# Performance work log

Hardware: AMD Instinct MI355X
Metric: run time of the kernel (lower is better)

The kernel has to match this reference:

```python
import jax, jax.numpy as jnp
import numpy as np

N_LAYERS = 3
FEATS = 128
POS = 3
M_DIM = 64
E_IN = 1 + 2 * FEATS          # 257 (rel_dist + x_i + x_j)
N_NODES = 20000
N_EDGES = 320000
LN_EPS = 1e-5


def _xavier(key, shape):
    fan_in, fan_out = shape[0], shape[1]
    std = (2.0 / (fan_in + fan_out)) ** 0.5
    return jax.random.normal(key, shape, dtype=jnp.float32) * std


def setup_inputs() -> dict:
    key = jax.random.key(0)
    ks = jax.random.split(key, 10)
    x = jax.random.normal(ks[0], (N_NODES, POS + FEATS), dtype=jnp.float32)
    edge_index = jax.random.randint(ks[1], (2, N_EDGES), 0, N_NODES)
    L = N_LAYERS
    def stack(k, shape):
        return jax.vmap(lambda kk: _xavier(kk, shape))(jax.random.split(k, L))
    params = {
        "ew1": stack(ks[2], (E_IN, 2 * E_IN)),      # edge_mlp linear 1
        "eb1": jnp.zeros((L, 2 * E_IN), jnp.float32),
        "ew2": stack(ks[3], (2 * E_IN, M_DIM)),      # edge_mlp linear 2
        "eb2": jnp.zeros((L, M_DIM), jnp.float32),
        "ng": jnp.ones((L, FEATS), jnp.float32),     # node LayerNorm gamma
        "nb": jnp.zeros((L, FEATS), jnp.float32),    # node LayerNorm beta
        "nw1": stack(ks[4], (FEATS + M_DIM, 2 * FEATS)),
        "nb1": jnp.zeros((L, 2 * FEATS), jnp.float32),
        "nw2": stack(ks[5], (2 * FEATS, FEATS)),
        "nb2": jnp.zeros((L, FEATS), jnp.float32),
        "cw1": stack(ks[6], (M_DIM, 4 * M_DIM)),
        "cb1": jnp.zeros((L, 4 * M_DIM), jnp.float32),
        "cw2": stack(ks[7], (4 * M_DIM, 1)),
        "cb2": jnp.zeros((L, 1), jnp.float32),
    }
    return {"x": x, "edge_index": edge_index, **params}


def _layer(x, edge_index, ew1, eb1, ew2, eb2, ng, nb, nw1, nb1, nw2, nb2,
           cw1, cb1, cw2, cb2):
    coors, feats = x[:, :POS], x[:, POS:]
    src, dst = edge_index[0], edge_index[1]
    # relative geometry per edge
    rel_coors = coors[src] - coors[dst]                       # [E, 3]
    rel_dist = jnp.sum(rel_coors * rel_coors, axis=-1, keepdims=True)  # [E, 1]
    # message MLP: cat[x_i (target), x_j (source), rel_dist]
    e_in = jnp.concatenate([feats[dst], feats[src], rel_dist], axis=-1)
    h = jax.nn.silu(e_in @ ew1 + eb1)
    m_ij = jax.nn.silu(h @ ew2 + eb2)                         # [E, m_dim]
    # coordinate update
    coor_w = jax.nn.silu(m_ij @ cw1 + cb1) @ cw2 + cb2        # [E, 1]
    mhat = jax.ops.segment_sum(coor_w * rel_coors, dst, num_segments=N_NODES)
    coors_out = coors + mhat
    # feature update (LayerNorm then MLP, residual)
    m_i = jax.ops.segment_sum(m_ij, dst, num_segments=N_NODES)
    mu = jnp.mean(feats, axis=-1, keepdims=True)
    var = jnp.mean((feats - mu) ** 2, axis=-1, keepdims=True)
    feats_n = (feats - mu) * jax.lax.rsqrt(var + LN_EPS) * ng + nb
    n_in = jnp.concatenate([feats_n, m_i], axis=-1)
    nh = jax.nn.silu(n_in @ nw1 + nb1) @ nw2 + nb2
    feats_out = feats + nh
    return jnp.concatenate([coors_out, feats_out], axis=-1)


def reference(x, edge_index, ew1, eb1, ew2, eb2, ng, nb, nw1, nb1, nw2, nb2,
              cw1, cb1, cw2, cb2):
    for l in range(N_LAYERS):
        x = _layer(x, edge_index,
                   ew1[l], eb1[l], ew2[l], eb2[l],
                   ng[l], nb[l], nw1[l], nb1[l], nw2[l], nb2[l],
                   cw1[l], cb1[l], cw2[l], cb2[l])
    return x
```

## Files before the change

kernel.cpp:

```cpp
#include <hip/hip_runtime.h>

typedef unsigned short u16;
typedef unsigned int   u32;
typedef __attribute__((ext_vector_type(2))) u32  u32x2;
typedef __attribute__((ext_vector_type(4))) u32  u32x4;
typedef __attribute__((ext_vector_type(8))) __bf16 bf16x8;
typedef __attribute__((ext_vector_type(4))) float  f32x4;

#define NN 20000
#define NE 320000
#define XD 131
#define F  128
#define MD 64
#define H1 514
#define H1P 544
#define NCH 17

#define GAS __attribute__((address_space(1)))
#define LAS __attribute__((address_space(3)))
#define LGKM0 asm volatile("s_waitcnt lgkmcnt(0)" ::: "memory")
#define VM0   asm volatile("s_waitcnt vmcnt(0)" ::: "memory")

__device__ __forceinline__ float silu(float a) {
    float e = __expf(-a);
    return a * __builtin_amdgcn_rcpf(1.0f + e);
}

__device__ __forceinline__ u16 f2bf(float f) {
    u32 u = __builtin_bit_cast(u32, f);
    return (u16)((u + 0x7FFFu + ((u >> 16) & 1u)) >> 16);
}
__device__ __forceinline__ u16 bfc(float f) { return __builtin_bit_cast(u16, (__bf16)f); }
__device__ __forceinline__ u32 pk2(float a, float b) {
    return (u32)bfc(a) | ((u32)bfc(b) << 16);
}
__device__ __forceinline__ float blo(u32 u) { return __builtin_bit_cast(float, u << 16); }
__device__ __forceinline__ float bhi(u32 u) { return __builtin_bit_cast(float, u & 0xFFFF0000u); }
__device__ __forceinline__ bf16x8 mk8(u32 a, u32 b, u32 c, u32 d) {
    u32x4 t = {a, b, c, d};
    return __builtin_bit_cast(bf16x8, t);
}
__device__ __forceinline__ f32x4 mfma16(bf16x8 a, bf16x8 b, f32x4 c) {
    return __builtin_amdgcn_mfma_f32_16x16x32_bf16(a, b, c, 0, 0, 0);
}


__global__ void prep_w1o(const float* __restrict__ ew1, const float* __restrict__ eb1,
                         u16* __restrict__ w1b, float* __restrict__ bias2) {
    int i = blockIdx.x * 256 + threadIdx.x;
    if (i >= 3 * H1P * 256) return;
    int k = i & 255;
    int n = (i >> 8) % H1P;
    int l = (i >> 8) / H1P;
    float v = (n < H1) ? ew1[(size_t)l * 257 * H1 + (size_t)k * H1 + n] : 0.f;
    w1b[(size_t)(l * H1P + n) * 256 + (k ^ ((n & 7) << 3))] = f2bf(v);
    if (k == 0) {
        bias2[(l * H1P + n) * 2 + 0] = (n < H1) ? eb1[l * H1 + n] : 0.f;
        bias2[(l * H1P + n) * 2 + 1] = (n < H1) ? ew1[(size_t)l * 257 * H1 + (size_t)256 * H1 + n] : 0.f;
    }
}

__global__ void prep_w1n(const float* __restrict__ ew1, const float* __restrict__ eb1,
                         u16* __restrict__ w1p, float* __restrict__ eb1p, float* __restrict__ w1lf) {
    int i = blockIdx.x * 256 + threadIdx.x;
    if (i >= 3 * 1088 * 128) return;
    int k = i & 127;
    int n = (i >> 7) % 1088;
    int l = (i >> 7) / 1088;
    float v;
    if (n < H1P) v = (n < H1) ? ew1[(size_t)l * 257 * H1 + (size_t)k * H1 + n] : 0.f;
    else { int nn = n - H1P; v = (nn < H1) ? ew1[(size_t)l * 257 * H1 + (size_t)(128 + k) * H1 + nn] : 0.f; }
    w1p[(size_t)(l * 1088 + n) * 128 + k] = f2bf(v);
    if (k == 0 && n < H1P) {
        eb1p[l * H1P + n] = (n < H1) ? eb1[l * H1 + n] : 0.f;
        w1lf[l * H1P + n] = (n < H1) ? ew1[(size_t)l * 257 * H1 + (size_t)256 * H1 + n] : 0.f;
    }
}

__global__ void prep_w2(const float* __restrict__ ew2, u16* __restrict__ w2b) {
    int i = blockIdx.x * 256 + threadIdx.x;
    if (i >= 3 * 64 * H1P) return;
    int k = i % H1P;
    int n = (i / H1P) & 63;
    int l = i / (H1P * 64);
    float v = (k < H1) ? ew2[(size_t)l * H1 * 64 + (size_t)k * 64 + n] : 0.f;
    w2b[(size_t)(l * 64 + n) * H1P + k] = f2bf(v);
}

__global__ void prep_cw1(const float* __restrict__ cw1, u16* __restrict__ cw1b) {
    int i = blockIdx.x * 256 + threadIdx.x;
    if (i >= 3 * 256 * 64) return;
    int k = i & 63;
    int n = (i >> 6) & 255;
    int l = i >> 14;
    cw1b[(size_t)l * 16384 + n * 64 + k] = f2bf(cw1[(size_t)l * 16384 + k * 256 + n]);
}

__global__ void prep_nw1(const float* __restrict__ nw1, u16* __restrict__ nw1b) {
    int i = blockIdx.x * 256 + threadIdx.x;
    if (i >= 3 * 256 * 192) return;
    int k = i % 192;
    int n = (i / 192) & 255;
    int l = i / (192 * 256);
    nw1b[(size_t)(l * 256 + n) * 192 + k] = f2bf(nw1[(size_t)l * 192 * 256 + (size_t)k * 256 + n]);
}

__global__ void prep_nw2(const float* __restrict__ nw2, u16* __restrict__ nw2b) {
    int i = blockIdx.x * 256 + threadIdx.x;
    if (i >= 3 * 128 * 256) return;
    int k = i & 255;
    int n = (i >> 8) & 127;
    int l = i >> 15;
    nw2b[(size_t)(l * 128 + n) * 256 + k] = f2bf(nw2[(size_t)l * 256 * 128 + (size_t)k * 128 + n]);
}

__global__ void x2bf(const float* __restrict__ xc, u32* __restrict__ xbf) {
    int i = blockIdx.x * 256 + threadIdx.x;
    if (i >= NN * 64) return;
    const int node = i >> 6, p = i & 63;
    const float a = xc[(size_t)node * XD + 3 + 2 * p];
    const float b = xc[(size_t)node * XD + 4 + 2 * p];
    xbf[(size_t)node * 64 + p] = pk2(a, b);
}


__global__ __launch_bounds__(256, 4) void ygemm(
    const u16* __restrict__ xbf, const char* __restrict__ w1p,
    const float* __restrict__ eb1p, u16* __restrict__ Y)
{
    const int tid = threadIdx.x;
    const int w = tid >> 6, l = tid & 63, lg = l >> 4, lc = l & 15;
    const int nb0 = blockIdx.x * 128 + w * 32;
    const int n0 = nb0 + lc, n1 = nb0 + 16 + lc;
    const bool v0 = n0 < NN, v1 = n1 < NN;
    const int m0 = v0 ? n0 : NN - 1, m1 = v1 ? n1 : NN - 1;

    bf16x8 BF[2][4];
    #pragma unroll
    for (int kt = 0; kt < 4; ++kt) {
        BF[0][kt] = *(const bf16x8*)((const char*)xbf + (size_t)m0 * 256 + kt * 64 + lg * 16);
        BF[1][kt] = *(const bf16x8*)((const char*)xbf + (size_t)m1 * 256 + kt * 64 + lg * 16);
    }

    const int t0 = blockIdx.y * 17;
    #pragma unroll 1
    for (int t = t0; t < t0 + 17; ++t) {
        bf16x8 AW[4];
        #pragma unroll
        for (int kt = 0; kt < 4; ++kt)
            AW[kt] = *(const bf16x8*)(w1p + (size_t)(t * 16 + lc) * 256 + kt * 64 + lg * 16);
        const int cb = t * 16 + lg * 4;
        f32x4 binit = {0.f, 0.f, 0.f, 0.f};
        if (cb < H1P) binit = *(const f32x4*)(eb1p + cb);
        f32x4 c0 = binit, c1 = binit;
        #pragma unroll
        for (int kt = 0; kt < 4; ++kt) {
            c0 = mfma16(AW[kt], BF[0][kt], c0);
            c1 = mfma16(AW[kt], BF[1][kt], c1);
        }
        u32x2 p0, p1;
        p0[0] = pk2(c0[0], c0[1]); p0[1] = pk2(c0[2], c0[3]);
        p1[0] = pk2(c1[0], c1[1]); p1[1] = pk2(c1[2], c1[3]);
        if (v0) *(u32x2*)(Y + (size_t)m0 * 1088 + cb) = p0;
        if (v1) *(u32x2*)(Y + (size_t)m1 * 1088 + cb) = p1;
    }
}


__global__ void csr_hist(const int* __restrict__ eidx, int* __restrict__ cnt) {
    int e = blockIdx.x * 256 + threadIdx.x;
    if (e < NE) atomicAdd(&cnt[eidx[NE + e]], 1);
}

__global__ void csr_scan(const int* __restrict__ cnt, int* __restrict__ rowp) {
    __shared__ int ps[1024];
    const int t = threadIdx.x;
    const int base = t * 20;
    int loc[20];
    int s = 0;
    #pragma unroll
    for (int i = 0; i < 20; ++i) {
        const int idx = base + i;
        const int c = (idx < NN) ? cnt[idx] : 0;
        loc[i] = s;
        s += c;
    }
    ps[t] = s;
    __syncthreads();
    for (int off = 1; off < 1024; off <<= 1) {
        int v = (t >= off) ? ps[t - off] : 0;
        __syncthreads();
        ps[t] += v;
        __syncthreads();
    }
    const int segbase = (t > 0) ? ps[t - 1] : 0;
    #pragma unroll
    for (int i = 0; i < 20; ++i) {
        const int idx = base + i;
        if (idx < NN) rowp[idx] = segbase + loc[i];
    }
    if (t == 1023) rowp[NN] = ps[1023];
}

__global__ void csr_fill(const int* __restrict__ eidx, const int* __restrict__ rowp,
                         int* __restrict__ fill, int* __restrict__ eids) {
    int e = blockIdx.x * 256 + threadIdx.x;
    if (e >= NE) return;
    const int d = eidx[NE + e];
    const int pos = atomicAdd(&fill[d], 1);
    eids[rowp[d] + pos] = e;
}

__global__ void esort(const int* __restrict__ eidx, const int* __restrict__ eids,
                      int* __restrict__ esrc, int* __restrict__ edst) {
    int j = blockIdx.x * 256 + threadIdx.x;
    if (j >= NE) return;
    const int e = eids[j];
    esrc[j] = eidx[e];
    edst[j] = eidx[NE + e];
}


__global__ __launch_bounds__(256, 4) void reduce_mi(
    const u16* __restrict__ gmij, const float* __restrict__ gmh,
    const int* __restrict__ rowp, float* __restrict__ m_i, float* __restrict__ mh) {
    const int tid = threadIdx.x;
    const int n = blockIdx.x * 8 + (tid >> 5);
    const int t = tid & 31;
    if (n >= NN) return;
    const int b = rowp[n], e = rowp[n + 1];
    float a0 = 0.f, a1 = 0.f;
    for (int j = b; j < e; ++j) {
        const u32 v = *(const u32*)(gmij + (size_t)j * 64 + t * 2);
        a0 += blo(v);
        a1 += bhi(v);
    }
    m_i[(size_t)n * 64 + 2 * t]     = a0;
    m_i[(size_t)n * 64 + 2 * t + 1] = a1;
    if (t < 3) {
        float m = 0.f;
        for (int j = b; j < e; ++j) m += gmh[(size_t)j * 4 + t];
        mh[n * 3 + t] = m;
    }
}


__global__ __launch_bounds__(256, 4) void edge_mfma2(
    const float* __restrict__ x, const u16* __restrict__ Y,
    const int* __restrict__ esrc, const int* __restrict__ edst,
    const float* __restrict__ w1lf,
    const char* __restrict__ w2b, const float* __restrict__ eb2,
    const char* __restrict__ cw1b, const float* __restrict__ cb1,
    const float* __restrict__ cw2, const float* __restrict__ cb2,
    u16* __restrict__ gmij, float* __restrict__ gmh)
{
    __shared__ __align__(16) char LDS[19456];
    const int tid = threadIdx.x;
    const int w = tid >> 6, l = tid & 63, lg = l >> 4, lc = l & 15;
    const int ebase = blockIdx.x * 128 + w * 32;
    char*  MJ  = LDS + w * 4352;
    float* RDS = (float*)(LDS + 17408);

    if (l < 32) {
        const int e = ebase + l;
        const int s = esrc[e], d = edst[e];
        const float ax = x[(size_t)s * XD + 0] - x[(size_t)d * XD + 0];
        const float ay = x[(size_t)s * XD + 1] - x[(size_t)d * XD + 1];
        const float az = x[(size_t)s * XD + 2] - x[(size_t)d * XD + 2];
        f32x4 v = {ax, ay, az, ax * ax + ay * ay + az * az};
        *(f32x4*)(RDS + (w * 32 + l) * 4) = v;
    }
    const int s0 = esrc[ebase + lc],      d0 = edst[ebase + lc];
    const int s1 = esrc[ebase + 16 + lc], d1 = edst[ebase + 16 + lc];
    LGKM0;
    const float rd0 = RDS[(w * 32 + lc) * 4 + 3];
    const float rd1 = RDS[(w * 32 + 16 + lc) * 4 + 3];

    f32x4 c2[2][4];
    #pragma unroll
    for (int nt = 0; nt < 4; ++nt) {
        const float b = eb2[nt * 16 + lc];
        c2[0][nt] = (f32x4){b, b, b, b};
        c2[1][nt] = (f32x4){b, b, b, b};
    }

    #pragma unroll 1
    for (int ch = 0; ch < NCH; ++ch) {
        const int cb = ch * 32 + lg * 8;
        u32x4 ya0 = *(const u32x4*)(Y + (size_t)d0 * 1088 + cb);
        u32x4 yb0 = *(const u32x4*)(Y + (size_t)s0 * 1088 + 544 + cb);
        u32x4 ya1 = *(const u32x4*)(Y + (size_t)d1 * 1088 + cb);
        u32x4 yb1 = *(const u32x4*)(Y + (size_t)s1 * 1088 + 544 + cb);
        f32x4 wlA = *(const f32x4*)(w1lf + cb);
        f32x4 wlB = *(const f32x4*)(w1lf + cb + 4);
        u32 pk0[4], pk1[4];
        #pragma unroll
        for (int j = 0; j < 4; ++j) {
            const float wa = (j < 2) ? wlA[2 * j]     : wlB[2 * j - 4];
            const float wb = (j < 2) ? wlA[2 * j + 1] : wlB[2 * j - 3];
            {
                const float a0 = blo(ya0[j]) + blo(yb0[j]) + rd0 * wa;
                const float a1 = bhi(ya0[j]) + bhi(yb0[j]) + rd0 * wb;
                pk0[j] = pk2(silu(a0), silu(a1));
            }
            {
                const float a0 = blo(ya1[j]) + blo(yb1[j]) + rd1 * wa;
                const float a1 = bhi(ya1[j]) + bhi(yb1[j]) + rd1 * wb;
                pk1[j] = pk2(silu(a0), silu(a1));
            }
        }
        bf16x8 A20 = mk8(pk0[0], pk0[1], pk0[2], pk0[3]);
        bf16x8 A21 = mk8(pk1[0], pk1[1], pk1[2], pk1[3]);
        #pragma unroll
        for (int nt = 0; nt < 4; ++nt) {
            bf16x8 Bw = __builtin_bit_cast(bf16x8,
                *(const u32x4*)(w2b + (size_t)(nt * 16 + lc) * 1088 + ch * 64 + lg * 16));
            c2[0][nt] = mfma16(A20, Bw, c2[0][nt]);
            c2[1][nt] = mfma16(A21, Bw, c2[1][nt]);
        }
    }

    #pragma unroll
    for (int mt = 0; mt < 2; ++mt)
        #pragma unroll
        for (int nt = 0; nt < 4; ++nt)
            #pragma unroll
            for (int r = 0; r < 4; ++r) {
                const float v = silu(c2[mt][nt][r]);
                const int rowl = mt * 16 + lg * 4 + r;
                const int col  = nt * 16 + lc;
                *(u16*)(MJ + rowl * 136 + col * 2) = bfc(v);
            }
    LGKM0;

    {
        u16* grow = gmij + (size_t)ebase * 64;
        #pragma unroll
        for (int i = 0; i < 4; ++i) {
            const int row = i * 8 + (l >> 3);
            u32x4 v = *(u32x4*)(MJ + row * 136 + (l & 7) * 16);
            *(u32x4*)(grow + (size_t)row * 64 + (l & 7) * 8) = v;
        }
    }

    bf16x8 A3[2][2];
    #pragma unroll
    for (int mt = 0; mt < 2; ++mt)
        #pragma unroll
        for (int kt = 0; kt < 2; ++kt)
            A3[mt][kt] = *(bf16x8*)(MJ + (mt * 16 + lc) * 136 + kt * 64 + lg * 16);

    float pw[2][4] = {{0.f, 0.f, 0.f, 0.f}, {0.f, 0.f, 0.f, 0.f}};
    #pragma unroll 4
    for (int ct3 = 0; ct3 < 16; ++ct3) {
        const int col = ct3 * 16 + lc;
        const float b = cb1[col];
        f32x4 c30 = {b, b, b, b}, c31 = {b, b, b, b};
        #pragma unroll
        for (int kt = 0; kt < 2; ++kt) {
            bf16x8 B = __builtin_bit_cast(bf16x8,
                *(const u32x4*)(cw1b + (size_t)col * 128 + kt * 64 + lg * 16));
            c30 = mfma16(A3[0][kt], B, c30);
            c31 = mfma16(A3[1][kt], B, c31);
        }
        const float w2v = cw2[col];
        #pragma unroll
        for (int r = 0; r < 4; ++r) {
            pw[0][r] = fmaf(silu(c30[r]), w2v, pw[0][r]);
            pw[1][r] = fmaf(silu(c31[r]), w2v, pw[1][r]);
        }
    }
    #pragma unroll
    for (int m = 1; m < 16; m <<= 1)
        #pragma unroll
        for (int mt = 0; mt < 2; ++mt)
            #pragma unroll
            for (int r = 0; r < 4; ++r)
                pw[mt][r] += __shfl_xor(pw[mt][r], m, 64);

    const float cb2v = cb2[0];
    if (lc < 3) {
        #pragma unroll
        for (int mt = 0; mt < 2; ++mt)
            #pragma unroll
            for (int r = 0; r < 4; ++r) {
                const int rowl = mt * 16 + lg * 4 + r;
                const float cwv = pw[mt][r] + cb2v;
                gmh[(size_t)(ebase + rowl) * 4 + lc] = cwv * RDS[(w * 32 + rowl) * 4 + lc];
            }
    }
}


__global__ __launch_bounds__(256, 3) void edge_mfma(
    const float* __restrict__ x, const u16* __restrict__ xbf,
    const int* __restrict__ esrc, const int* __restrict__ edst,
    const char* __restrict__ w1b, const float* __restrict__ bias2,
    const char* __restrict__ w2b, const float* __restrict__ eb2,
    const char* __restrict__ cw1b, const float* __restrict__ cb1,
    const float* __restrict__ cw2, const float* __restrict__ cb2,
    float* __restrict__ m_i, float* __restrict__ mhat,
    u16* __restrict__ gmij, float* __restrict__ gmh)
{
    __shared__ __align__(16) char LDS[45568];
    const int tid = threadIdx.x;
    const int w = tid >> 6, l = tid & 63, lg = l >> 4, lc = l & 15;
    const int ebase = blockIdx.x * 128 + w * 32;
    char*  HT  = LDS + 32768 + w * 2560;
    char*  MJ  = LDS + w * 4352;
    float* RDS = (float*)(LDS + 43008);
    int*   SDS = (int*)(LDS + 45056);
    char*  STG = LDS + w * 8192;

    if (l < 32) {
        const int e = ebase + l;
        const int s = esrc[e], d = edst[e];
        const float ax = x[(size_t)s * XD + 0] - x[(size_t)d * XD + 0];
        const float ay = x[(size_t)s * XD + 1] - x[(size_t)d * XD + 1];
        const float az = x[(size_t)s * XD + 2] - x[(size_t)d * XD + 2];
        f32x4 v = {ax, ay, az, ax * ax + ay * ay + az * az};
        *(f32x4*)(RDS + (w * 32 + l) * 4) = v;
        SDS[w * 32 + l] = d;
    }

    bf16x8 A[2][8];
    const int r4 = l >> 4;
    #pragma unroll
    for (int p = 0; p < 2; ++p) {
        const int* ea = p ? esrc : edst;
        #pragma unroll
        for (int j = 0; j < 8; ++j) {
            const int r = j * 4 + r4;
            const int node = ea[ebase + r];
            const int cp = lc ^ (r & 7);
            __builtin_amdgcn_global_load_lds((const GAS u32*)(xbf + (size_t)node * 128 + cp * 8),
                                             (LAS u32*)(STG + j * 1024), 16, 0, 0);
        }
        VM0;
        #pragma unroll
        for (int kt = 0; kt < 4; ++kt)
            #pragma unroll
            for (int et = 0; et < 2; ++et) {
                const int R = et * 16 + lc;
                A[et][p * 4 + kt] = *(bf16x8*)(STG + R * 256 + ((kt * 64 + lg * 16) ^ ((R & 7) << 4)));
            }
        LGKM0;
    }

    float rd_e[2];
    rd_e[0] = RDS[(w * 32 + lc) * 4 + 3];
    rd_e[1] = RDS[(w * 32 + 16 + lc) * 4 + 3];
    LGKM0;

    __syncthreads();

    f32x4 c2[2][4];
    #pragma unroll
    for (int nt = 0; nt < 4; ++nt) {
        const float b = eb2[nt * 16 + lc];
        c2[0][nt] = (f32x4){b, b, b, b};
        c2[1][nt] = (f32x4){b, b, b, b};
    }

    {
        const char* g = w1b + (size_t)w * 4096;
        #pragma unroll
        for (int r = 0; r < 4; ++r)
            __builtin_amdgcn_global_load_lds((const GAS u32*)(g + r * 1024 + l * 16),
                                             (LAS u32*)(LDS + w * 4096 + r * 1024), 16, 0, 0);
    }

    const float* pB = bias2;
    #pragma unroll 1
    for (int ch = 0; ch < NCH; ++ch) {
        VM0;
        __syncthreads();
        if (ch + 1 < NCH) {
            const char* g = w1b + (size_t)(ch + 1) * 16384 + w * 4096;
            char* dst = LDS + ((ch + 1) & 1) * 16384 + w * 4096;
            #pragma unroll
            for (int r = 0; r < 4; ++r)
                __builtin_amdgcn_global_load_lds((const GAS u32*)(g + r * 1024 + l * 16),
                                                 (LAS u32*)(dst + r * 1024), 16, 0, 0);
        }
        char* Bc = LDS + (ch & 1) * 16384;

        #pragma unroll
        for (int nt = 0; nt < 2; ++nt) {
            const float* bp = pB + (nt * 16 + lg * 4) * 2;
            f32x4 q0 = *(const f32x4*)(bp);
            f32x4 q1 = *(const f32x4*)(bp + 4);
            f32x4 c10, c11;
            c10[0] = fmaf(rd_e[0], q0[1], q0[0]); c10[1] = fmaf(rd_e[0], q0[3], q0[2]);
            c10[2] = fmaf(rd_e[0], q1[1], q1[0]); c10[3] = fmaf(rd_e[0], q1[3], q1[2]);
            c11[0] = fmaf(rd_e[1], q0[1], q0[0]); c11[1] = fmaf(rd_e[1], q0[3], q0[2]);
            c11[2] = fmaf(rd_e[1], q1[1], q1[0]); c11[3] = fmaf(rd_e[1], q1[3], q1[2]);
            const int nl = nt * 16 + lc;
            #pragma unroll
            for (int kt = 0; kt < 8; ++kt) {
                bf16x8 Wf = *(bf16x8*)(Bc + nl * 512 + ((kt * 64 + lg * 16) ^ ((nl & 7) << 4)));
                c10 = mfma16(Wf, A[0][kt], c10);
                c11 = mfma16(Wf, A[1][kt], c11);
            }
            u32x2 v0, v1;
            v0[0] = pk2(silu(c10[0]), silu(c10[1])); v0[1] = pk2(silu(c10[2]), silu(c10[3]));
            v1[0] = pk2(silu(c11[0]), silu(c11[1])); v1[1] = pk2(silu(c11[2]), silu(c11[3]));
            *(u32x2*)(HT + lc * 80 + nt * 32 + lg * 8) = v0;
            *(u32x2*)(HT + (16 + lc) * 80 + nt * 32 + lg * 8) = v1;
        }
        LGKM0;
        bf16x8 A2[2];
        A2[0] = *(bf16x8*)(HT + lc * 80 + lg * 16);
        A2[1] = *(bf16x8*)(HT + (16 + lc) * 80 + lg * 16);
        #pragma unroll
        for (int nt = 0; nt < 4; ++nt) {
            bf16x8 Bw = __builtin_bit_cast(bf16x8,
                *(const u32x4*)(w2b + (size_t)(nt * 16 + lc) * 1088 + ch * 64 + lg * 16));
            c2[0][nt] = mfma16(A2[0], Bw, c2[0][nt]);
            c2[1][nt] = mfma16(A2[1], Bw, c2[1][nt]);
        }
        pB += 64;
    }

    __syncthreads();

    int dstn[2][4];
    #pragma unroll
    for (int mt = 0; mt < 2; ++mt)
        #pragma unroll
        for (int r = 0; r < 4; ++r)
            dstn[mt][r] = SDS[w * 32 + mt * 16 + lg * 4 + r];

    #pragma unroll
    for (int mt = 0; mt < 2; ++mt)
        #pragma unroll
        for (int nt = 0; nt < 4; ++nt)
            #pragma unroll
            for (int r = 0; r < 4; ++r) {
                const float v = silu(c2[mt][nt][r]);
                const int rowl = mt * 16 + lg * 4 + r;
                const int col  = nt * 16 + lc;
                *(u16*)(MJ + rowl * 136 + col * 2) = bfc(v);
                if (!gmij) atomicAdd(m_i + (size_t)dstn[mt][r] * 64 + col, v);
            }
    LGKM0;

    if (gmij) {
        u16* grow = gmij + (size_t)ebase * 64;
        #pragma unroll
        for (int i = 0; i < 4; ++i) {
            const int row = i * 8 + (l >> 3);
            u32x4 v = *(u32x4*)(MJ + row * 136 + (l & 7) * 16);
            *(u32x4*)(grow + (size_t)row * 64 + (l & 7) * 8) = v;
        }
    }

    bf16x8 A3[2][2];
    #pragma unroll
    for (int mt = 0; mt < 2; ++mt)
        #pragma unroll
        for (int kt = 0; kt < 2; ++kt)
            A3[mt][kt] = *(bf16x8*)(MJ + (mt * 16 + lc) * 136 + kt * 64 + lg * 16);

    float pw[2][4] = {{0.f, 0.f, 0.f, 0.f}, {0.f, 0.f, 0.f, 0.f}};
    #pragma unroll 4
    for (int ct3 = 0; ct3 < 16; ++ct3) {
        const int col = ct3 * 16 + lc;
        const float b = cb1[col];
        f32x4 c30 = {b, b, b, b}, c31 = {b, b, b, b};
        #pragma unroll
        for (int kt = 0; kt < 2; ++kt) {
            bf16x8 B = __builtin_bit_cast(bf16x8,
                *(const u32x4*)(cw1b + (size_t)col * 128 + kt * 64 + lg * 16));
            c30 = mfma16(A3[0][kt], B, c30);
            c31 = mfma16(A3[1][kt], B, c31);
        }
        const float w2v = cw2[col];
        #pragma unroll
        for (int r = 0; r < 4; ++r) {
            pw[0][r] = fmaf(silu(c30[r]), w2v, pw[0][r]);
            pw[1][r] = fmaf(silu(c31[r]), w2v, pw[1][r]);
        }
    }
    #pragma unroll
    for (int m = 1; m < 16; m <<= 1)
        #pragma unroll
        for (int mt = 0; mt < 2; ++mt)
            #pragma unroll
            for (int r = 0; r < 4; ++r)
                pw[mt][r] += __shfl_xor(pw[mt][r], m, 64);

    const float cb2v = cb2[0];
    if (lc < 3) {
        #pragma unroll
        for (int mt = 0; mt < 2; ++mt)
            #pragma unroll
            for (int r = 0; r < 4; ++r) {
                const int rowl = mt * 16 + lg * 4 + r;
                const float cwv = pw[mt][r] + cb2v;
                const float contrib = cwv * RDS[(w * 32 + rowl) * 4 + lc];
                if (gmij)
                    gmh[(size_t)(ebase + rowl) * 4 + lc] = contrib;
                else
                    atomicAdd(mhat + (size_t)dstn[mt][r] * 3 + lc, contrib);
            }
    }
}


__global__ __launch_bounds__(256, 2) void node_mfma(
    const float* __restrict__ xc, const float* __restrict__ m_i, const float* __restrict__ mh,
    const float* __restrict__ ng, const float* __restrict__ nb,
    const char* __restrict__ nw1b, const float* __restrict__ nb1,
    const char* __restrict__ nw2b, const float* __restrict__ nb2,
    float* __restrict__ xn)
{
    __shared__ __align__(16) char LDS[4 * 4352];
    const int tid = threadIdx.x;
    const int w = tid >> 6, l = tid & 63, lg = l >> 4, lc = l & 15;
    char* HB = LDS + w * 4352;
    const int nb0 = blockIdx.x * 128 + w * 32;

    int nodes[2]; bool valid[2];
    #pragma unroll
    for (int et = 0; et < 2; ++et) {
        int n = nb0 + et * 16 + lc;
        valid[et] = (n < NN);
        nodes[et] = valid[et] ? n : (NN - 1);
    }

    bf16x8 BF[2][6];
    #pragma unroll
    for (int et = 0; et < 2; ++et) {
        const float* xr = xc + (size_t)nodes[et] * XD + 3;
        float v[4][8];
        float s = 0.f, q = 0.f;
        #pragma unroll
        for (int kt = 0; kt < 4; ++kt) {
            const int k0 = kt * 32 + lg * 8;
            #pragma unroll
            for (int j = 0; j < 8; ++j) {
                const float t = xr[k0 + j];
                v[kt][j] = t; s += t; q = fmaf(t, t, q);
            }
        }
        s += __shfl_xor(s, 16, 64); s += __shfl_xor(s, 32, 64);
        q += __shfl_xor(q, 16, 64); q += __shfl_xor(q, 32, 64);
        const float mu = s * (1.f / 128.f);
        const float rs = rsqrtf(q * (1.f / 128.f) - mu * mu + 1e-5f);
        #pragma unroll
        for (int kt = 0; kt < 4; ++kt) {
            const int k0 = kt * 32 + lg * 8;
            float4 g0 = *(const float4*)(ng + k0), g1 = *(const float4*)(ng + k0 + 4);
            float4 b0 = *(const float4*)(nb + k0), b1 = *(const float4*)(nb + k0 + 4);
            const u32 u0 = pk2((v[kt][0] - mu) * rs * g0.x + b0.x, (v[kt][1] - mu) * rs * g0.y + b0.y);
            const u32 u1 = pk2((v[kt][2] - mu) * rs * g0.z + b0.z, (v[kt][3] - mu) * rs * g0.w + b0.w);
            const u32 u2 = pk2((v[kt][4] - mu) * rs * g1.x + b1.x, (v[kt][5] - mu) * rs * g1.y + b1.y);
            const u32 u3 = pk2((v[kt][6] - mu) * rs * g1.z + b1.z, (v[kt][7] - mu) * rs * g1.w + b1.w);
            BF[et][kt] = mk8(u0, u1, u2, u3);
        }
        const float* mr = m_i + (size_t)nodes[et] * 64;
        #pragma unroll
        for (int kt2 = 0; kt2 < 2; ++kt2) {
            float4 a = *(const float4*)(mr + kt2 * 32 + lg * 8);
            float4 b = *(const float4*)(mr + kt2 * 32 + lg * 8 + 4);
            BF[et][4 + kt2] = mk8(pk2(a.x, a.y), pk2(a.z, a.w), pk2(b.x, b.y), pk2(b.z, b.w));
        }
    }

    f32x4 a2[8][2];
    #pragma unroll
    for (int ct2 = 0; ct2 < 8; ++ct2) {
        f32x4 b = *(const f32x4*)(nb2 + ct2 * 16 + lg * 4);
        a2[ct2][0] = b; a2[ct2][1] = b;
    }

    #pragma unroll 1
    for (int g = 0; g < 4; ++g) {
        f32x4 a1[4][2];
        #pragma unroll
        for (int ct = 0; ct < 4; ++ct) {
            f32x4 b = *(const f32x4*)(nb1 + g * 64 + ct * 16 + lg * 4);
            a1[ct][0] = b; a1[ct][1] = b;
        }
        #pragma unroll
        for (int ct = 0; ct < 4; ++ct)
            #pragma unroll
            for (int kt = 0; kt < 6; ++kt) {
                bf16x8 Aw = __builtin_bit_cast(bf16x8, *(const u32x4*)(
                    nw1b + (size_t)(g * 64 + ct * 16 + lc) * 384 + kt * 64 + lg * 16));
                a1[ct][0] = mfma16(Aw, BF[0][kt], a1[ct][0]);
                a1[ct][1] = mfma16(Aw, BF[1][kt], a1[ct][1]);
            }
        #pragma unroll
        for (int ct = 0; ct < 4; ++ct)
            #pragma unroll
            for (int et = 0; et < 2; ++et) {
                f32x4 c = a1[ct][et];
                u32 v0 = pk2(silu(c[0]), silu(c[1]));
                u32 v1 = pk2(silu(c[2]), silu(c[3]));
                *(u32*)(HB + (et * 16 + lc) * 136 + ct * 32 + lg * 8) = v0;
                *(u32*)(HB + (et * 16 + lc) * 136 + ct * 32 + lg * 8 + 4) = v1;
            }
        LGKM0;
        __builtin_amdgcn_sched_barrier(0);
        bf16x8 B2[2][2];
        #pragma unroll
        for (int et = 0; et < 2; ++et)
            #pragma unroll
            for (int kt2 = 0; kt2 < 2; ++kt2) {
                u32 a = *(u32*)(HB + (et * 16 + lc) * 136 + kt2 * 64 + lg * 16);
                u32 b = *(u32*)(HB + (et * 16 + lc) * 136 + kt2 * 64 + lg * 16 + 4);
                u32 c = *(u32*)(HB + (et * 16 + lc) * 136 + kt2 * 64 + lg * 16 + 8);
                u32 d = *(u32*)(HB + (et * 16 + lc) * 136 + kt2 * 64 + lg * 16 + 12);
                B2[et][kt2] = mk8(a, b, c, d);
            }
        #pragma unroll
        for (int ct2 = 0; ct2 < 8; ++ct2)
            #pragma unroll
            for (int kt2 = 0; kt2 < 2; ++kt2) {
                bf16x8 Aw = __builtin_bit_cast(bf16x8, *(const u32x4*)(
                    nw2b + (size_t)(ct2 * 16 + lc) * 512 + (g * 64 + kt2 * 32 + lg * 8) * 2));
                a2[ct2][0] = mfma16(Aw, B2[0][kt2], a2[ct2][0]);
                a2[ct2][1] = mfma16(Aw, B2[1][kt2], a2[ct2][1]);
            }
        LGKM0;
        __builtin_amdgcn_sched_barrier(0);
    }

    #pragma unroll
    for (int et = 0; et < 2; ++et) {
        if (!valid[et]) continue;
        const size_t nr = (size_t)nodes[et] * XD;
        #pragma unroll
        for (int ct2 = 0; ct2 < 8; ++ct2)
            #pragma unroll
            for (int r = 0; r < 4; ++r) {
                const int col = ct2 * 16 + lg * 4 + r;
                xn[nr + 3 + col] = a2[ct2][et][r] + xc[nr + 3 + col];
            }
    }
    for (int idx = tid; idx < 384; idx += 256) {
        const int n = blockIdx.x * 128 + idx / 3;
        const int d = idx - (idx / 3) * 3;
        if (n < NN)
            xn[(size_t)n * XD + d] = xc[(size_t)n * XD + d] + mh[n * 3 + d];
    }
}


extern "C" void kernel_launch(void* const* d_in, const int* in_sizes, int n_in,
                              void* d_out, int out_size, void* d_ws, size_t ws_size,
                              hipStream_t stream) {
    const float* x_in = (const float*)d_in[0];
    const int*   eidx = (const int*)  d_in[1];
    const float* ew1  = (const float*)d_in[2];
    const float* eb1  = (const float*)d_in[3];
    const float* ew2  = (const float*)d_in[4];
    const float* eb2  = (const float*)d_in[5];
    const float* ng   = (const float*)d_in[6];
    const float* nb   = (const float*)d_in[7];
    const float* nw1  = (const float*)d_in[8];
    const float* nb1  = (const float*)d_in[9];
    const float* nw2  = (const float*)d_in[10];
    const float* nb2  = (const float*)d_in[11];
    const float* cw1  = (const float*)d_in[12];
    const float* cb1  = (const float*)d_in[13];
    const float* cw2  = (const float*)d_in[14];
    const float* cb2  = (const float*)d_in[15];
    float* out = (float*)d_out;

    char* ws = (char*)d_ws;
    size_t off = 0;
    auto alloc = [&](size_t bytes) { char* p = ws + off; off = (off + bytes + 255) & ~255ull; return p; };
    float* mi    = (float*)alloc((size_t)NN * MD * 4);
    float* mh    = (float*)alloc((size_t)NN * 3 * 4);
    u32*   xbf   = (u32*)  alloc((size_t)NN * 256);
    float* bias2 = (float*)alloc((size_t)3 * H1P * 8);
    float* eb1pf = (float*)alloc((size_t)3 * H1P * 4);
    float* w1lf  = (float*)alloc((size_t)3 * H1P * 4);
    char*  w1b   = alloc((size_t)3 * H1P * 512);
    char*  w1p   = alloc((size_t)3 * 1088 * 256);
    char*  w2b   = alloc((size_t)3 * 64 * 1088);
    char*  cw1b  = alloc((size_t)3 * 256 * 128);
    char*  nw1b  = alloc((size_t)3 * 256 * 384);
    char*  nw2b  = alloc((size_t)3 * 128 * 512);
    int* rowp = (int*) alloc((size_t)(NN + 1) * 4);
    int* eids = (int*) alloc((size_t)NE * 4);
    int* esrc = (int*) alloc((size_t)NE * 4);
    int* edst = (int*) alloc((size_t)NE * 4);
    int* cnt  = (int*) alloc((size_t)NN * 4);
    int* fillp= (int*) alloc((size_t)NN * 4);
    u16* gmij = (u16*)alloc((size_t)NE * 64 * 2);
    float* gmh= (float*)alloc((size_t)NE * 4 * 4);
    const size_t off_two = off;
    u16* Ybuf = (u16*)alloc((size_t)NN * 1088 * 2);
    const size_t off_all = off;
    const bool pathA = (off_all <= ws_size);
    const bool two   = (off_two <= ws_size);

    prep_w1o<<<(3 * H1P * 256 + 255) / 256, 256, 0, stream>>>(ew1, eb1, (u16*)w1b, bias2);
    prep_w1n<<<(3 * 1088 * 128 + 255) / 256, 256, 0, stream>>>(ew1, eb1, (u16*)w1p, eb1pf, w1lf);
    prep_w2 <<<(3 * 64 * H1P + 255) / 256, 256, 0, stream>>>(ew2, (u16*)w2b);
    prep_cw1<<<(3 * 256 * 64 + 255) / 256, 256, 0, stream>>>(cw1, (u16*)cw1b);
    prep_nw1<<<(3 * 256 * 192 + 255) / 256, 256, 0, stream>>>(nw1, (u16*)nw1b);
    prep_nw2<<<(3 * 128 * 256 + 255) / 256, 256, 0, stream>>>(nw2, (u16*)nw2b);

    const int* esrcA = eidx;
    const int* edstA = eidx + NE;
    if (two) {
        hipMemsetAsync(cnt,  0, (size_t)NN * 4, stream);
        hipMemsetAsync(fillp,0, (size_t)NN * 4, stream);
        csr_hist<<<(NE + 255) / 256, 256, 0, stream>>>(eidx, cnt);
        csr_scan<<<1, 1024, 0, stream>>>(cnt, rowp);
        csr_fill<<<(NE + 255) / 256, 256, 0, stream>>>(eidx, rowp, fillp, eids);
        esort<<<(NE + 255) / 256, 256, 0, stream>>>(eidx, eids, esrc, edst);
        esrcA = esrc; edstA = edst;
    }

    for (int l = 0; l < 3; ++l) {
        const float* xc = (l == 0) ? x_in : out;
        float*       xn = out;
        if (!two) {
            hipMemsetAsync(mi, 0, (size_t)NN * MD * 4, stream);
            hipMemsetAsync(mh, 0, (size_t)NN * 3 * 4, stream);
        }
        x2bf<<<(NN * 64 + 255) / 256, 256, 0, stream>>>(xc, xbf);
        if (pathA) {
            ygemm<<<dim3((NN + 127) / 128, 4), 256, 0, stream>>>(
                (const u16*)xbf, w1p + (size_t)l * 1088 * 256, eb1pf + (size_t)l * H1P, Ybuf);
            edge_mfma2<<<NE / 128, 256, 0, stream>>>(
                xc, Ybuf, esrcA, edstA, w1lf + (size_t)l * H1P,
                w2b + (size_t)l * 64 * 1088, eb2 + (size_t)l * 64,
                cw1b + (size_t)l * 256 * 128, cb1 + (size_t)l * 256,
                cw2 + (size_t)l * 256, cb2 + l, gmij, gmh);
            reduce_mi<<<(NN + 7) / 8, 256, 0, stream>>>(gmij, gmh, rowp, mi, mh);
        } else {
            edge_mfma<<<NE / 128, 256, 0, stream>>>(
                xc, (const u16*)xbf, esrcA, edstA,
                w1b + (size_t)l * H1P * 512, bias2 + (size_t)l * H1P * 2,
                w2b + (size_t)l * 64 * 1088, eb2 + (size_t)l * 64,
                cw1b + (size_t)l * 256 * 128, cb1 + (size_t)l * 256,
                cw2 + (size_t)l * 256, cb2 + l,
                mi, mh, two ? gmij : (u16*)nullptr, two ? gmh : (float*)nullptr);
            if (two)
                reduce_mi<<<(NN + 7) / 8, 256, 0, stream>>>(gmij, gmh, rowp, mi, mh);
        }
        node_mfma<<<(NN + 127) / 128, 256, 0, stream>>>(
            xc, mi, mh,
            ng + (size_t)l * F, nb + (size_t)l * F,
            nw1b + (size_t)l * 256 * 384, nb1 + (size_t)l * 256,
            nw2b + (size_t)l * 128 * 512, nb2 + (size_t)l * F,
            xn);
    }
}
```

Baseline: 821.3 us.

## Prefetch next Y chunk in edge kernel and swizzle blocks across XCDs

```diff
diff --git a/kernel.cpp b/kernel.cpp
--- a/kernel.cpp
+++ b/kernel.cpp
@@ -123,7 +123,6 @@
     xbf[(size_t)node * 64 + p] = pk2(a, b);
 }
 
-
 __global__ __launch_bounds__(256, 4) void ygemm(
     const u16* __restrict__ xbf, const char* __restrict__ w1p,
     const float* __restrict__ eb1p, u16* __restrict__ Y)
@@ -257,7 +256,10 @@
     __shared__ __align__(16) char LDS[19456];
     const int tid = threadIdx.x;
     const int w = tid >> 6, l = tid & 63, lg = l >> 4, lc = l & 15;
-    const int ebase = blockIdx.x * 128 + w * 32;
+    const int bx = blockIdx.x;
+    const int xcd = bx & 7, ib = bx >> 3;
+    const int swb = (xcd < 4 ? xcd * 313 : 1252 + (xcd - 4) * 312) + ib;
+    const int ebase = swb * 128 + w * 32;
     char*  MJ  = LDS + w * 4352;
     float* RDS = (float*)(LDS + 17408);
 
@@ -284,15 +286,29 @@
         c2[1][nt] = (f32x4){b, b, b, b};
     }
 
+    const u16* ya0p = Y + (size_t)d0 * 1088;
+    const u16* yb0p = Y + (size_t)s0 * 1088 + 544;
+    const u16* ya1p = Y + (size_t)d1 * 1088;
+    const u16* yb1p = Y + (size_t)s1 * 1088 + 544;
+    const int co = lg * 8;
+
+    u32x4 ya0 = *(const u32x4*)(ya0p + co);
+    u32x4 yb0 = *(const u32x4*)(yb0p + co);
+    u32x4 ya1 = *(const u32x4*)(ya1p + co);
+    u32x4 yb1 = *(const u32x4*)(yb1p + co);
+    f32x4 wlA = *(const f32x4*)(w1lf + co);
+    f32x4 wlB = *(const f32x4*)(w1lf + co + 4);
+
     #pragma unroll 1
     for (int ch = 0; ch < NCH; ++ch) {
-        const int cb = ch * 32 + lg * 8;
-        u32x4 ya0 = *(const u32x4*)(Y + (size_t)d0 * 1088 + cb);
-        u32x4 yb0 = *(const u32x4*)(Y + (size_t)s0 * 1088 + 544 + cb);
-        u32x4 ya1 = *(const u32x4*)(Y + (size_t)d1 * 1088 + cb);
-        u32x4 yb1 = *(const u32x4*)(Y + (size_t)s1 * 1088 + 544 + cb);
-        f32x4 wlA = *(const f32x4*)(w1lf + cb);
-        f32x4 wlB = *(const f32x4*)(w1lf + cb + 4);
+        const int cn = (ch + 1 < NCH) ? (ch + 1) * 32 + co : co;
+        u32x4 na0 = *(const u32x4*)(ya0p + cn);
+        u32x4 nb0 = *(const u32x4*)(yb0p + cn);
+        u32x4 na1 = *(const u32x4*)(ya1p + cn);
+        u32x4 nb1 = *(const u32x4*)(yb1p + cn);
+        f32x4 nwA = *(const f32x4*)(w1lf + cn);
+        f32x4 nwB = *(const f32x4*)(w1lf + cn + 4);
+
         u32 pk0[4], pk1[4];
         #pragma unroll
         for (int j = 0; j < 4; ++j) {
@@ -318,6 +334,7 @@
             c2[0][nt] = mfma16(A20, Bw, c2[0][nt]);
             c2[1][nt] = mfma16(A21, Bw, c2[1][nt]);
         }
+        ya0 = na0; yb0 = nb0; ya1 = na1; yb1 = nb1; wlA = nwA; wlB = nwB;
     }
 
     #pragma unroll
```

Measured after the change: 836.1 us. No clear change (+1.8%).
